# Kernel optimization log

Measured on AMD Instinct MI355X. Metric: run time of the kernel, lower is better.

The kernel has to match this reference:

```python
import jax, jax.numpy as jnp
import numpy as np

NUM_HEADS = 8
NORM_GROUPS = 32
EPS = 1e-5


def setup_inputs() -> dict:
    key = jax.random.key(0)
    k1, k2, k3 = jax.random.split(key, 3)
    b, c, h, w = 16, 256, 64, 64
    x = jax.random.normal(k1, (b, c, h, w), dtype=jnp.float32)
    gn_w = jnp.ones((c,), dtype=jnp.float32)
    gn_b = jnp.zeros((c,), dtype=jnp.float32)
    # 1x1 convs == channel matmuls; init like torch (kaiming-ish scale)
    w_qkv = jax.random.normal(k2, (3 * c, c), dtype=jnp.float32) / np.sqrt(c)
    w_proj = jax.random.normal(k3, (c, c), dtype=jnp.float32) / np.sqrt(c)
    b_proj = jnp.zeros((c,), dtype=jnp.float32)
    return {"x": x, "gn_w": gn_w, "gn_b": gn_b, "w_qkv": w_qkv,
            "w_proj": w_proj, "b_proj": b_proj}


def reference(x, gn_w, gn_b, w_qkv, w_proj, b_proj):
    b, c, h, w = x.shape
    H = NUM_HEADS
    d = c // H
    n = h * w
    # GroupNorm over (channels_per_group, h, w)
    xg = x.reshape(b, NORM_GROUPS, -1)
    mu = jnp.mean(xg, axis=-1, keepdims=True)
    var = jnp.mean(jnp.square(xg - mu), axis=-1, keepdims=True)
    xn = ((xg - mu) * jax.lax.rsqrt(var + EPS)).reshape(b, c, h, w)
    xn = xn * gn_w[None, :, None, None] + gn_b[None, :, None, None]
    # 1x1 conv -> (b, 3c, h, w); channel layout is (qkv, heads, d)
    qkv = jnp.einsum('oc,bchw->bohw', w_qkv, xn)
    qkv = qkv.reshape(b, 3, H, d, n)
    q, k, v = qkv[:, 0], qkv[:, 1], qkv[:, 2]  # each (b, H, d, n)
    k = jax.nn.softmax(k, axis=-1)
    # linear attention: small (d x d) state per head
    att = jnp.einsum('bhdn,bhen->bhde', k, v)
    out = jnp.einsum('bhde,bhdn->bhen', att, q)  # (b, H, d, n)
    out = out.reshape(b, c, h, w)
    return jnp.einsum('oc,bchw->bohw', w_proj, out) + b_proj[None, :, None, None]
```

## Files before the change

kernel.cpp:

```cpp
#include <hip/hip_runtime.h>
#include <stdint.h>

#define BATCH 16
#define CCH   256
#define NSP   4096

typedef unsigned short u16;
typedef short  short8 __attribute__((ext_vector_type(8)));
typedef float  f32x4  __attribute__((ext_vector_type(4)));

__device__ __forceinline__ float bf2f(u16 h) {
  union { unsigned int u; float f; } x; x.u = ((unsigned int)h) << 16; return x.f;
}
__device__ __forceinline__ u16 f2bf(float f) {
  union { float f; unsigned int u; } x; x.f = f;
  unsigned int r = 0x7fffu + ((x.u >> 16) & 1u);
  return (u16)((x.u + r) >> 16);
}

#define GLB(p) ((__attribute__((address_space(1))) void*)(p))
#define LDSP(p) ((__attribute__((address_space(3))) void*)(p))

__global__ __launch_bounds__(256) void prep_kernel(const float* __restrict__ x,
                                                   const float* __restrict__ wq,
                                                   const float* __restrict__ wp,
                                                   float2* __restrict__ stats,
                                                   float* __restrict__ att4,
                                                   u16* __restrict__ wbf,
                                                   u16* __restrict__ wqT) {
  __shared__ float red[8];
  __shared__ u16 ls[64][72];
  const int blk = blockIdx.x, tid = threadIdx.x;
  if (blk < 512) {
    {
      float* az = att4 + (size_t)blk * 264;
      for (int i = tid; i < 264; i += 256) az[i] = 0.f;
    }
    const float4* xv = (const float4*)(x + (size_t)blk * 32768);
    float s = 0.f, ss = 0.f;
    for (int i = tid; i < 8192; i += 256) {
      float4 u = xv[i];
      s  += u.x + u.y + u.z + u.w;
      ss += u.x * u.x + u.y * u.y + u.z * u.z + u.w * u.w;
    }
#pragma unroll
    for (int off = 32; off > 0; off >>= 1) {
      s  += __shfl_down(s, off);
      ss += __shfl_down(ss, off);
    }
    const int wave = tid >> 6, lane = tid & 63;
    if (lane == 0) { red[wave * 2] = s; red[wave * 2 + 1] = ss; }
    __syncthreads();
    if (tid == 0) {
      const float S  = red[0] + red[2] + red[4] + red[6];
      const float SS = red[1] + red[3] + red[5] + red[7];
      const float mean = S * (1.f / 32768.f);
      const float var  = SS * (1.f / 32768.f) - mean * mean;
      stats[blk] = make_float2(mean, rsqrtf(var + 1e-5f));
    }
  } else if (blk < 768) {
    const int i = ((blk - 512) * 256 + tid) * 4;
    float4 v = (i < 196608) ? *(const float4*)(wq + i)
                            : *(const float4*)(wp + (i - 196608));
    ushort4 o;
    o.x = f2bf(v.x); o.y = f2bf(v.y); o.z = f2bf(v.z); o.w = f2bf(v.w);
    *(ushort4*)(wbf + i) = o;
  } else {
    const int t2 = blk - 768;
    const int c0 = (t2 & 3) * 64, r0 = (t2 >> 2) * 64;
#pragma unroll
    for (int j = 0; j < 4; ++j) {
      const int row = j * 16 + (tid >> 4), col = (tid & 15) * 4;
      float4 u = *(const float4*)(wq + (r0 + row) * 256 + c0 + col);
      ls[row][col]     = f2bf(u.x);
      ls[row][col + 1] = f2bf(u.y);
      ls[row][col + 2] = f2bf(u.z);
      ls[row][col + 3] = f2bf(u.w);
    }
    __syncthreads();
#pragma unroll
    for (int j = 0; j < 2; ++j) {
      const int crow = j * 32 + (tid >> 3), d8 = (tid & 7) * 8;
      u16 tmp[8];
#pragma unroll
      for (int k = 0; k < 8; ++k) tmp[k] = ls[d8 + k][crow];
      *(uint4*)(wqT + (c0 + crow) * 256 + r0 + d8) = *(uint4*)tmp;
    }
  }
}

__global__ __launch_bounds__(256) void gn_apply_t(const float* __restrict__ x,
                                                  const float* __restrict__ gw,
                                                  const float* __restrict__ gb,
                                                  const float2* __restrict__ stats,
                                                  u16* __restrict__ xnT) {
  __shared__ u16 ls[64][72];
  const int b = blockIdx.z, c0 = blockIdx.y * 64, n0 = blockIdx.x * 64;
  const int tid = threadIdx.x;
#pragma unroll
  for (int r = 0; r < 4; ++r) {
    const int cc = (tid >> 4) + r * 16;
    const int nn = (tid & 15) * 4;
    const int c = c0 + cc;
    const float2 st = stats[b * 32 + (c >> 3)];
    const float wv = gw[c] * st.y;
    const float bv = gb[c] - st.x * wv;
    float4 u = *(const float4*)(x + ((size_t)b * CCH + c) * NSP + n0 + nn);
    ushort4 o;
    o.x = f2bf(u.x * wv + bv);
    o.y = f2bf(u.y * wv + bv);
    o.z = f2bf(u.z * wv + bv);
    o.w = f2bf(u.w * wv + bv);
    *(ushort4*)&ls[cc][nn] = o;
  }
  __syncthreads();
#pragma unroll
  for (int p = 0; p < 2; ++p) {
    const int idx = tid + p * 256;
    const int nn = idx >> 3;
    const int cb = (idx & 7) * 8;
    u16 tmp[8];
#pragma unroll
    for (int j = 0; j < 8; ++j) tmp[j] = ls[cb + j][nn];
    *(uint4*)(xnT + ((size_t)b * NSP + n0 + nn) * CCH + c0 + cb) = *(uint4*)tmp;
  }
}

template <int OUTF32>
__global__ __launch_bounds__(256) void gemm_mfma(const u16* __restrict__ A,
                                                 const u16* __restrict__ Bt,
                                                 const float* __restrict__ bias,
                                                 void* __restrict__ Cm, int M,
                                                 int aBatch, long btStride, int ldc) {
  __shared__ __align__(16) u16 smem[17408];
  const int tid = threadIdx.x, wave = tid >> 6, lane = tid & 63;
  const int n0 = blockIdx.x * 128, m0 = blockIdx.y * 128, bz = blockIdx.z;
  const u16* Ab = A + (size_t)bz * aBatch;
  const u16* Bb = Bt + (size_t)bz * btStride;

  const int lrow = lane >> 3;
  const int kcl  = ((lane & 7) ^ lrow) * 8;
  const u16* pA[4]; const u16* pB[4];
#pragma unroll
  for (int j = 0; j < 4; ++j) {
    const int row = j * 32 + wave * 8 + lrow;
    pA[j] = Ab + (size_t)(m0 + row) * CCH + kcl;
    pB[j] = Bb + (size_t)(n0 + row) * CCH + kcl;
  }
  u16* lA = smem;
  u16* lB = smem + 8192;

  const int wm = wave >> 1, wn = wave & 1;
  f32x4 acc[4][4];
#pragma unroll
  for (int i = 0; i < 4; ++i)
#pragma unroll
    for (int j = 0; j < 4; ++j) acc[i][j] = (f32x4){0.f, 0.f, 0.f, 0.f};

  for (int it = 0; it < 4; ++it) {
#pragma unroll
    for (int j = 0; j < 4; ++j) {
      __builtin_amdgcn_global_load_lds(GLB(pA[j]), LDSP(lA + (j * 256 + wave * 64) * 8), 16, 0, 0);
      __builtin_amdgcn_global_load_lds(GLB(pB[j]), LDSP(lB + (j * 256 + wave * 64) * 8), 16, 0, 0);
      pA[j] += 64; pB[j] += 64;
    }
    __syncthreads();
#pragma unroll
    for (int w = 0; w < 2; ++w) {
      const int kcf = w * 4 + (lane >> 4);
      short8 af[4], bfr[4];
#pragma unroll
      for (int mt = 0; mt < 4; ++mt) {
        const int row = wm * 64 + mt * 16 + (lane & 15);
        af[mt] = *(const short8*)&lA[(row * 8 + (kcf ^ (row & 7))) * 8];
      }
#pragma unroll
      for (int nt = 0; nt < 4; ++nt) {
        const int row = wn * 64 + nt * 16 + (lane & 15);
        bfr[nt] = *(const short8*)&lB[(row * 8 + (kcf ^ (row & 7))) * 8];
      }
#pragma unroll
      for (int mt = 0; mt < 4; ++mt)
#pragma unroll
        for (int nt = 0; nt < 4; ++nt)
          acc[mt][nt] = __builtin_amdgcn_mfma_f32_16x16x32_bf16(af[mt], bfr[nt], acc[mt][nt], 0, 0, 0);
    }
    __syncthreads();
  }

  if (!OUTF32) {
    u16* cl = smem;
#pragma unroll
    for (int mt = 0; mt < 4; ++mt)
#pragma unroll
      for (int nt = 0; nt < 4; ++nt)
#pragma unroll
        for (int r = 0; r < 4; ++r) {
          const int row = wm * 64 + mt * 16 + (lane >> 4) * 4 + r;
          const int col = wn * 64 + nt * 16 + (lane & 15);
          cl[row * 136 + col] = f2bf(acc[mt][nt][r]);
        }
    __syncthreads();
    u16* C = (u16*)Cm + (size_t)bz * (size_t)M * ldc;
#pragma unroll
    for (int j = 0; j < 8; ++j) {
      const int idx = tid + j * 256;
      const int row = idx >> 4, chunk = idx & 15;
      *(uint4*)(C + (size_t)(m0 + row) * ldc + n0 + chunk * 8) =
          *(const uint4*)&cl[row * 136 + chunk * 8];
    }
  } else {
    float* clf = (float*)smem;
    float* C = (float*)Cm + (size_t)bz * (size_t)M * ldc;
#pragma unroll
    for (int pass = 0; pass < 2; ++pass) {
      if (wm == pass) {
#pragma unroll
        for (int mt = 0; mt < 4; ++mt)
#pragma unroll
          for (int nt = 0; nt < 4; ++nt)
#pragma unroll
            for (int r = 0; r < 4; ++r) {
              const int rl = mt * 16 + (lane >> 4) * 4 + r;
              const int col = wn * 64 + nt * 16 + (lane & 15);
              clf[rl * 132 + col] = acc[mt][nt][r] + bias[m0 + pass * 64 + rl];
            }
      }
      __syncthreads();
#pragma unroll
      for (int j = 0; j < 8; ++j) {
        const int idx = tid + j * 256;
        const int row = idx >> 5, chunk = idx & 31;
        *(float4*)(C + (size_t)(m0 + pass * 64 + row) * ldc + n0 + chunk * 4) =
            *(const float4*)&clf[row * 132 + chunk * 4];
      }
      __syncthreads();
    }
  }
}

__global__ __launch_bounds__(256, 4) void gemm_kv_att(const u16* __restrict__ A,
                                                      const u16* __restrict__ Bt,
                                                      float* __restrict__ att4) {
  __shared__ __align__(16) u16 smem[17408];
  const int tid = threadIdx.x, wave = tid >> 6, lane = tid & 63;
  const int n0 = blockIdx.x * 128, hg = blockIdx.y, b = blockIdx.z;
  const u16* Bb = Bt + (size_t)b * (size_t)NSP * CCH;

  const int lrow = lane >> 3;
  const int kcl  = ((lane & 7) ^ lrow) * 8;
  const u16* pA[4]; const u16* pB[4];
#pragma unroll
  for (int j = 0; j < 4; ++j) {
    const int arow = 256 + (j >> 1) * 256 + hg * 64 + (j & 1) * 32 + wave * 8 + lrow;
    pA[j] = A  + (size_t)arow * CCH + kcl;
    pB[j] = Bb + (size_t)(n0 + j * 32 + wave * 8 + lrow) * CCH + kcl;
  }
  u16* lA = smem;
  u16* lB = smem + 8192;

  const int wm = wave >> 1, wn = wave & 1;
  f32x4 acc[4][4];
#pragma unroll
  for (int i = 0; i < 4; ++i)
#pragma unroll
    for (int j = 0; j < 4; ++j) acc[i][j] = (f32x4){0.f, 0.f, 0.f, 0.f};

  for (int it = 0; it < 4; ++it) {
#pragma unroll
    for (int j = 0; j < 4; ++j) {
      __builtin_amdgcn_global_load_lds(GLB(pA[j]), LDSP(lA + (j * 256 + wave * 64) * 8), 16, 0, 0);
      __builtin_amdgcn_global_load_lds(GLB(pB[j]), LDSP(lB + (j * 256 + wave * 64) * 8), 16, 0, 0);
      pA[j] += 64; pB[j] += 64;
    }
    __syncthreads();
#pragma unroll
    for (int w = 0; w < 2; ++w) {
      const int kcf = w * 4 + (lane >> 4);
      short8 af[4], bfr[4];
#pragma unroll
      for (int mt = 0; mt < 4; ++mt) {
        const int row = wm * 64 + mt * 16 + (lane & 15);
        af[mt] = *(const short8*)&lA[(row * 8 + (kcf ^ (row & 7))) * 8];
      }
#pragma unroll
      for (int nt = 0; nt < 4; ++nt) {
        const int row = wn * 64 + nt * 16 + (lane & 15);
        bfr[nt] = *(const short8*)&lB[(row * 8 + (kcf ^ (row & 7))) * 8];
      }
#pragma unroll
      for (int mt = 0; mt < 4; ++mt)
#pragma unroll
        for (int nt = 0; nt < 4; ++nt)
          acc[mt][nt] = __builtin_amdgcn_mfma_f32_16x16x32_bf16(af[mt], bfr[nt], acc[mt][nt], 0, 0, 0);
    }
    __syncthreads();
  }

  u16* clK = smem;
  u16* clV = smem + 8704;
  {
    const int rbase = (lane >> 4) * 4;
    if (wm == 0) {
#pragma unroll
      for (int mt = 0; mt < 4; ++mt)
#pragma unroll
        for (int nt = 0; nt < 4; ++nt)
#pragma unroll
          for (int r = 0; r < 4; ++r) {
            const int row = mt * 16 + rbase + r;
            const int col = wn * 64 + nt * 16 + (lane & 15);
            clK[row * 136 + col] = f2bf(__expf(acc[mt][nt][r]));
          }
    } else {
#pragma unroll
      for (int mt = 0; mt < 4; ++mt)
#pragma unroll
        for (int nt = 0; nt < 4; ++nt)
#pragma unroll
          for (int r = 0; r < 4; ++r) {
            const int row = mt * 16 + rbase + r;
            const int col = wn * 64 + nt * 16 + (lane & 15);
            clV[row * 136 + col] = f2bf(acc[mt][nt][r]);
          }
    }
  }
  __syncthreads();

  const int hh = wave >> 1, nhalf = wave & 1;
  const int bh = b * 8 + hg * 2 + hh;
  f32x4 a2[2][2], al[2];
#pragma unroll
  for (int i = 0; i < 2; ++i) {
    al[i] = (f32x4){0.f, 0.f, 0.f, 0.f};
#pragma unroll
    for (int j = 0; j < 2; ++j) a2[i][j] = (f32x4){0.f, 0.f, 0.f, 0.f};
  }
  short8 ones;
#pragma unroll
  for (int j = 0; j < 8; ++j) ones[j] = (short)0x3F80;

  const int rr = lane & 15, cc8 = (lane >> 4) * 8;
#pragma unroll
  for (int c = 0; c < 2; ++c) {
    const int n = (nhalf * 2 + c) * 32 + cc8;
    short8 ek0 = *(const short8*)&clK[(hh * 32 + rr) * 136 + n];
    short8 ek1 = *(const short8*)&clK[(hh * 32 + 16 + rr) * 136 + n];
    short8 v0  = *(const short8*)&clV[(hh * 32 + rr) * 136 + n];
    short8 v1  = *(const short8*)&clV[(hh * 32 + 16 + rr) * 136 + n];
    a2[0][0] = __builtin_amdgcn_mfma_f32_16x16x32_bf16(ek0, v0, a2[0][0], 0, 0, 0);
    a2[0][1] = __builtin_amdgcn_mfma_f32_16x16x32_bf16(ek0, v1, a2[0][1], 0, 0, 0);
    a2[1][0] = __builtin_amdgcn_mfma_f32_16x16x32_bf16(ek1, v0, a2[1][0], 0, 0, 0);
    a2[1][1] = __builtin_amdgcn_mfma_f32_16x16x32_bf16(ek1, v1, a2[1][1], 0, 0, 0);
    al[0]    = __builtin_amdgcn_mfma_f32_16x16x32_bf16(ek0, ones, al[0], 0, 0, 0);
    al[1]    = __builtin_amdgcn_mfma_f32_16x16x32_bf16(ek1, ones, al[1], 0, 0, 0);
  }
  __syncthreads();

  float* red  = (float*)smem;
  float* redl = red + 2176;
  const int dq = (lane >> 4) * 4;
  if (nhalf == 1) {
#pragma unroll
    for (int dh = 0; dh < 2; ++dh) {
#pragma unroll
      for (int eh = 0; eh < 2; ++eh)
#pragma unroll
        for (int j = 0; j < 4; ++j)
          red[hh * 1088 + (dh * 16 + dq + j) * 34 + eh * 16 + rr] = a2[dh][eh][j];
      if (rr == 0)
#pragma unroll
        for (int j = 0; j < 4; ++j) redl[hh * 32 + dh * 16 + dq + j] = al[dh][j];
    }
  }
  __syncthreads();
  if (nhalf == 0) {
    float* ap = att4 + (size_t)bh * 1056;
#pragma unroll
    for (int dh = 0; dh < 2; ++dh) {
#pragma unroll
      for (int eh = 0; eh < 2; ++eh)
#pragma unroll
        for (int j = 0; j < 4; ++j) {
          const int d = dh * 16 + dq + j, e = eh * 16 + rr;
          atomicAdd(&ap[d * 32 + e], a2[dh][eh][j] + red[hh * 1088 + d * 34 + e]);
        }
      if (rr == 0)
#pragma unroll
        for (int j = 0; j < 4; ++j) {
          const int d = dh * 16 + dq + j;
          atomicAdd(&ap[1024 + d], al[dh][j] + redl[hh * 32 + d]);
        }
    }
  }
}

__global__ __launch_bounds__(256) void w2_kernel(const u16* __restrict__ wp_bf,
                                                 const float* __restrict__ att4,
                                                 u16* __restrict__ W2) {
  const int b = blockIdx.x >> 4;
  const int o0 = (blockIdx.x & 15) * 16;
  const int tid = threadIdx.x;
  const int h = tid >> 5, d = tid & 31;
  const float* ap = att4 + ((size_t)b * 8 + h) * 1056;
  const float linv = 1.f / ap[1024 + d];
  float as[32];
#pragma unroll
  for (int e = 0; e < 32; ++e) as[e] = ap[d * 32 + e] * linv;
  u16* w2p = W2 + (size_t)b * 65536;
  for (int oi = 0; oi < 16; ++oi) {
    const int o = o0 + oi;
    const uint4* wr = (const uint4*)(wp_bf + o * 256 + h * 32);
    float acc = 0.f;
#pragma unroll
    for (int j = 0; j < 4; ++j) {
      uint4 u = wr[j];
      const u16* w8 = (const u16*)&u;
#pragma unroll
      for (int t = 0; t < 8; ++t) acc += bf2f(w8[t]) * as[j * 8 + t];
    }
    w2p[o * 256 + tid] = f2bf(acc);
  }
}

extern "C" void kernel_launch(void* const* d_in, const int* in_sizes, int n_in,
                              void* d_out, int out_size, void* d_ws, size_t ws_size,
                              hipStream_t stream) {
  const float* x      = (const float*)d_in[0];
  const float* gn_w   = (const float*)d_in[1];
  const float* gn_b   = (const float*)d_in[2];
  const float* w_qkv  = (const float*)d_in[3];
  const float* w_proj = (const float*)d_in[4];
  const float* b_proj = (const float*)d_in[5];
  float* out = (float*)d_out;

  char* ws = (char*)d_ws;
  u16*    xnT   = (u16*)ws;
  u16*    wbf   = (u16*)(ws + 33554432ull);
  u16*    wqT   = (u16*)(ws + 34078720ull);
  u16*    W2    = (u16*)(ws + 34209792ull);
  u16*    W3    = (u16*)(ws + 36306944ull);
  float*  att4  = (float*)(ws + 38404096ull);
  float2* stats = (float2*)(ws + 38944768ull);
  u16* wq_bf = wbf;
  u16* wp_bf = wbf + 196608;

  prep_kernel<<<784, 256, 0, stream>>>(x, w_qkv, w_proj, stats, att4, wbf, wqT);
  gn_apply_t<<<dim3(64, 4, 16), 256, 0, stream>>>(x, gn_w, gn_b, stats, xnT);
  gemm_kv_att<<<dim3(32, 4, 16), 256, 0, stream>>>(wq_bf, xnT, att4);
  w2_kernel<<<256, 256, 0, stream>>>(wp_bf, att4, W2);
  gemm_mfma<0><<<dim3(2, 2, 16), 256, 0, stream>>>(W2, wqT, nullptr, W3,
                                                   CCH, 65536, 0L, CCH);
  gemm_mfma<1><<<dim3(32, 2, 16), 256, 0, stream>>>(W3, xnT, b_proj, out,
                                                    CCH, 65536, (long)NSP * CCH, NSP);
}
```

Before: 208.1 us.

## Fuse all stages into one persistent cooperative kernel with grid syncs

Wraps each stage body in a device function and adds a cooperative persistent kernel that runs all six phases in sequence, separated by grid-wide barriers. Blocks loop over each phase's tiles with a fixed grid of 1024. The goal is to remove kernel launch overhead and the inter-kernel drain gaps. In exchange it adds grid-sync cost, pins the occupancy assumption to 4 blocks per CU, and leaves most of the grid idle during the small phases. Non-cooperative launches remain as a fallback.

New measurement: 213.2 us. 1.02x slower.

```diff
diff --git a/kernel.cpp b/kernel.cpp
--- a/kernel.cpp
+++ b/kernel.cpp
@@ -1,5 +1,8 @@
 #include <hip/hip_runtime.h>
+#include <hip/hip_cooperative_groups.h>
 #include <stdint.h>
+
+namespace cg = cooperative_groups;
 
 #define BATCH 16
 #define CCH   256
@@ -21,17 +24,12 @@
 #define GLB(p) ((__attribute__((address_space(1))) void*)(p))
 #define LDSP(p) ((__attribute__((address_space(3))) void*)(p))
 
-__global__ __launch_bounds__(256) void prep_kernel(const float* __restrict__ x,
-                                                   const float* __restrict__ wq,
-                                                   const float* __restrict__ wp,
-                                                   float2* __restrict__ stats,
-                                                   float* __restrict__ att4,
-                                                   u16* __restrict__ wbf,
-                                                   u16* __restrict__ wqT) {
-  __shared__ float red[8];
-  __shared__ u16 ls[64][72];
-  const int blk = blockIdx.x, tid = threadIdx.x;
+__device__ __forceinline__ void prep_body(int blk, int tid, const float* x,
+                                          const float* wq, const float* wp,
+                                          float2* stats, float* att4,
+                                          u16* wbf, u16* wqT, u16* smem) {
   if (blk < 512) {
+    float* red = (float*)(smem + 4608);
     {
       float* az = att4 + (size_t)blk * 264;
       for (int i = tid; i < 264; i += 256) az[i] = 0.f;
@@ -66,6 +64,7 @@
     o.x = f2bf(v.x); o.y = f2bf(v.y); o.z = f2bf(v.z); o.w = f2bf(v.w);
     *(ushort4*)(wbf + i) = o;
   } else {
+    u16 (*ls)[72] = (u16(*)[72])smem;
     const int t2 = blk - 768;
     const int c0 = (t2 & 3) * 64, r0 = (t2 >> 2) * 64;
 #pragma unroll
@@ -89,14 +88,12 @@
   }
 }
 
-__global__ __launch_bounds__(256) void gn_apply_t(const float* __restrict__ x,
-                                                  const float* __restrict__ gw,
-                                                  const float* __restrict__ gb,
-                                                  const float2* __restrict__ stats,
-                                                  u16* __restrict__ xnT) {
-  __shared__ u16 ls[64][72];
-  const int b = blockIdx.z, c0 = blockIdx.y * 64, n0 = blockIdx.x * 64;
-  const int tid = threadIdx.x;
+__device__ __forceinline__ void gn_apply_body(int n0t, int c0t, int b, int tid,
+                                              const float* x, const float* gw,
+                                              const float* gb, const float2* stats,
+                                              u16* xnT, u16* smem) {
+  u16 (*ls)[72] = (u16(*)[72])smem;
+  const int c0 = c0t * 64, n0 = n0t * 64;
 #pragma unroll
   for (int r = 0; r < 4; ++r) {
     const int cc = (tid >> 4) + r * 16;
@@ -127,14 +124,12 @@
 }
 
 template <int OUTF32>
-__global__ __launch_bounds__(256) void gemm_mfma(const u16* __restrict__ A,
-                                                 const u16* __restrict__ Bt,
-                                                 const float* __restrict__ bias,
-                                                 void* __restrict__ Cm, int M,
-                                                 int aBatch, long btStride, int ldc) {
-  __shared__ __align__(16) u16 smem[17408];
-  const int tid = threadIdx.x, wave = tid >> 6, lane = tid & 63;
-  const int n0 = blockIdx.x * 128, m0 = blockIdx.y * 128, bz = blockIdx.z;
+__device__ __forceinline__ void gemm_body(const u16* A, const u16* Bt,
+                                          const float* bias, void* Cm, int M,
+                                          int aBatch, long btStride, int ldc,
+                                          int n0, int m0, int bz,
+                                          int tid, u16* smem) {
+  const int wave = tid >> 6, lane = tid & 63;
   const u16* Ab = A + (size_t)bz * aBatch;
   const u16* Bb = Bt + (size_t)bz * btStride;
 
@@ -239,12 +234,11 @@
   }
 }
 
-__global__ __launch_bounds__(256, 4) void gemm_kv_att(const u16* __restrict__ A,
-                                                      const u16* __restrict__ Bt,
-                                                      float* __restrict__ att4) {
-  __shared__ __align__(16) u16 smem[17408];
-  const int tid = threadIdx.x, wave = tid >> 6, lane = tid & 63;
-  const int n0 = blockIdx.x * 128, hg = blockIdx.y, b = blockIdx.z;
+__device__ __forceinline__ void kv_att_body(int nblk, int hg, int b, int tid,
+                                            const u16* A, const u16* Bt,
+                                            float* att4, u16* smem) {
+  const int wave = tid >> 6, lane = tid & 63;
+  const int n0 = nblk * 128;
   const u16* Bb = Bt + (size_t)b * (size_t)NSP * CCH;
 
   const int lrow = lane >> 3;
@@ -395,12 +389,10 @@
   }
 }
 
-__global__ __launch_bounds__(256) void w2_kernel(const u16* __restrict__ wp_bf,
-                                                 const float* __restrict__ att4,
-                                                 u16* __restrict__ W2) {
-  const int b = blockIdx.x >> 4;
-  const int o0 = (blockIdx.x & 15) * 16;
-  const int tid = threadIdx.x;
+__device__ __forceinline__ void w2_body(int blk, int tid, const u16* wp_bf,
+                                        const float* att4, u16* W2) {
+  const int b = blk >> 4;
+  const int o0 = (blk & 15) * 16;
   const int h = tid >> 5, d = tid & 31;
   const float* ap = att4 + ((size_t)b * 8 + h) * 1056;
   const float linv = 1.f / ap[1024 + d];
@@ -420,6 +412,105 @@
       for (int t = 0; t < 8; ++t) acc += bf2f(w8[t]) * as[j * 8 + t];
     }
     w2p[o * 256 + tid] = f2bf(acc);
+  }
+}
+
+__global__ __launch_bounds__(256) void prep_kernel(const float* __restrict__ x,
+                                                   const float* __restrict__ wq,
+                                                   const float* __restrict__ wp,
+                                                   float2* __restrict__ stats,
+                                                   float* __restrict__ att4,
+                                                   u16* __restrict__ wbf,
+                                                   u16* __restrict__ wqT) {
+  __shared__ __align__(16) u16 smem[17408];
+  prep_body(blockIdx.x, threadIdx.x, x, wq, wp, stats, att4, wbf, wqT, smem);
+}
+
+__global__ __launch_bounds__(256) void gn_apply_t(const float* __restrict__ x,
+                                                  const float* __restrict__ gw,
+                                                  const float* __restrict__ gb,
+                                                  const float2* __restrict__ stats,
+                                                  u16* __restrict__ xnT) {
+  __shared__ __align__(16) u16 smem[17408];
+  gn_apply_body(blockIdx.x, blockIdx.y, blockIdx.z, threadIdx.x, x, gw, gb, stats, xnT, smem);
+}
+
+template <int OUTF32>
+__global__ __launch_bounds__(256) void gemm_mfma(const u16* __restrict__ A,
+                                                 const u16* __restrict__ Bt,
+                                                 const float* __restrict__ bias,
+                                                 void* __restrict__ Cm, int M,
+                                                 int aBatch, long btStride, int ldc) {
+  __shared__ __align__(16) u16 smem[17408];
+  gemm_body<OUTF32>(A, Bt, bias, Cm, M, aBatch, btStride, ldc,
+                    blockIdx.x * 128, blockIdx.y * 128, blockIdx.z,
+                    threadIdx.x, smem);
+}
+
+__global__ __launch_bounds__(256, 4) void gemm_kv_att(const u16* __restrict__ A,
+                                                      const u16* __restrict__ Bt,
+                                                      float* __restrict__ att4) {
+  __shared__ __align__(16) u16 smem[17408];
+  kv_att_body(blockIdx.x, blockIdx.y, blockIdx.z, threadIdx.x, A, Bt, att4, smem);
+}
+
+__global__ __launch_bounds__(256) void w2_kernel(const u16* __restrict__ wp_bf,
+                                                 const float* __restrict__ att4,
+                                                 u16* __restrict__ W2) {
+  w2_body(blockIdx.x, threadIdx.x, wp_bf, att4, W2);
+}
+
+__global__ __launch_bounds__(256, 4) void fused_all(
+    const float* __restrict__ x, const float* __restrict__ gn_w,
+    const float* __restrict__ gn_b, const float* __restrict__ w_qkv,
+    const float* __restrict__ w_proj, const float* __restrict__ b_proj,
+    float* __restrict__ out, u16* __restrict__ xnT, u16* __restrict__ wbf,
+    u16* __restrict__ wqT, u16* __restrict__ W2, u16* __restrict__ W3,
+    float* __restrict__ att4, float2* __restrict__ stats) {
+  __shared__ __align__(16) u16 smem[17408];
+  cg::grid_group grid = cg::this_grid();
+  const int bid = blockIdx.x, tid = threadIdx.x;
+  const int g = gridDim.x;
+  const u16* wq_bf = wbf;
+  const u16* wp_bf = wbf + 196608;
+
+  for (int i = bid; i < 784; i += g) {
+    prep_body(i, tid, x, w_qkv, w_proj, stats, att4, wbf, wqT, smem);
+    __syncthreads();
+  }
+  __threadfence();
+  grid.sync();
+
+  for (int it = bid; it < 4096; it += g) {
+    gn_apply_body(it & 63, (it >> 6) & 3, it >> 8, tid, x, gn_w, gn_b, stats, xnT, smem);
+    __syncthreads();
+  }
+  __threadfence();
+  grid.sync();
+
+  for (int it = bid; it < 2048; it += g) {
+    kv_att_body(it & 31, (it >> 5) & 3, it >> 7, tid, wq_bf, xnT, att4, smem);
+    __syncthreads();
+  }
+  __threadfence();
+  grid.sync();
+
+  for (int i = bid; i < 256; i += g) w2_body(i, tid, wp_bf, att4, W2);
+  __threadfence();
+  grid.sync();
+
+  for (int i = bid; i < 64; i += g) {
+    gemm_body<0>(W2, wqT, nullptr, W3, CCH, 65536, 0L, CCH,
+                 (i & 1) * 128, ((i >> 1) & 1) * 128, i >> 2, tid, smem);
+    __syncthreads();
+  }
+  __threadfence();
+  grid.sync();
+
+  for (int it = bid; it < 1024; it += g) {
+    gemm_body<1>(W3, xnT, b_proj, out, CCH, 65536, (long)NSP * CCH, NSP,
+                 (it & 31) * 128, ((it >> 5) & 1) * 128, it >> 6, tid, smem);
+    __syncthreads();
   }
 }
 
@@ -445,6 +536,25 @@
   u16* wq_bf = wbf;
   u16* wp_bf = wbf + 196608;
 
+  static int coop_state = 0;
+  if (coop_state == 0) {
+    int occ = 0;
+    hipError_t e = hipOccupancyMaxActiveBlocksPerMultiprocessor(
+        &occ, (const void*)fused_all, 256, 0);
+    coop_state = (e == hipSuccess && occ >= 4) ? 1 : -1;
+  }
+  if (coop_state == 1) {
+    void* args[14] = {
+      (void*)&x, (void*)&gn_w, (void*)&gn_b, (void*)&w_qkv, (void*)&w_proj,
+      (void*)&b_proj, (void*)&out, (void*)&xnT, (void*)&wbf, (void*)&wqT,
+      (void*)&W2, (void*)&W3, (void*)&att4, (void*)&stats
+    };
+    hipError_t e = hipLaunchCooperativeKernel((void*)fused_all, dim3(1024),
+                                              dim3(256), args, 0, stream);
+    if (e == hipSuccess) return;
+    coop_state = -1;
+  }
+
   prep_kernel<<<784, 256, 0, stream>>>(x, w_qkv, w_proj, stats, att4, wbf, wqT);
   gn_apply_t<<<dim3(64, 4, 16), 256, 0, stream>>>(x, gn_w, gn_b, stats, xnT);
   gemm_kv_att<<<dim3(32, 4, 16), 256, 0, stream>>>(wq_bf, xnT, att4);
```

## Fuse W2 computation into the W3 GEMM kernel, removing a launch

Applied to the files above, without the earlier changes.

Merges w2_kernel and the bf16-output gemm into one w23_kernel. Each block normalizes the per-head attention state into LDS, builds its 128-row slice of W2 with MFMA directly in LDS, then multiplies by wqT to produce W3. This removes one kernel launch and the W2 round trip through global memory. In exchange each block recomputes its W2 rows, which duplicates that work across the column blocks, and the kernel uses much more shared memory.

New measurement: 214.3 us. 1.03x slower.

```diff
diff --git a/kernel.cpp b/kernel.cpp
--- a/kernel.cpp
+++ b/kernel.cpp
@@ -126,12 +126,11 @@
   }
 }
 
-template <int OUTF32>
-__global__ __launch_bounds__(256) void gemm_mfma(const u16* __restrict__ A,
-                                                 const u16* __restrict__ Bt,
-                                                 const float* __restrict__ bias,
-                                                 void* __restrict__ Cm, int M,
-                                                 int aBatch, long btStride, int ldc) {
+__global__ __launch_bounds__(256) void gemm_f32(const u16* __restrict__ A,
+                                                const u16* __restrict__ Bt,
+                                                const float* __restrict__ bias,
+                                                float* __restrict__ Cm, int M,
+                                                int aBatch, long btStride, int ldc) {
   __shared__ __align__(16) u16 smem[17408];
   const int tid = threadIdx.x, wave = tid >> 6, lane = tid & 63;
   const int n0 = blockIdx.x * 128, m0 = blockIdx.y * 128, bz = blockIdx.z;
@@ -188,54 +187,31 @@
     __syncthreads();
   }
 
-  if (!OUTF32) {
-    u16* cl = smem;
-#pragma unroll
-    for (int mt = 0; mt < 4; ++mt)
-#pragma unroll
-      for (int nt = 0; nt < 4; ++nt)
-#pragma unroll
-        for (int r = 0; r < 4; ++r) {
-          const int row = wm * 64 + mt * 16 + (lane >> 4) * 4 + r;
-          const int col = wn * 64 + nt * 16 + (lane & 15);
-          cl[row * 136 + col] = f2bf(acc[mt][nt][r]);
-        }
-    __syncthreads();
-    u16* C = (u16*)Cm + (size_t)bz * (size_t)M * ldc;
+  float* clf = (float*)smem;
+  float* C = Cm + (size_t)bz * (size_t)M * ldc;
+#pragma unroll
+  for (int pass = 0; pass < 2; ++pass) {
+    if (wm == pass) {
+#pragma unroll
+      for (int mt = 0; mt < 4; ++mt)
+#pragma unroll
+        for (int nt = 0; nt < 4; ++nt)
+#pragma unroll
+          for (int r = 0; r < 4; ++r) {
+            const int rl = mt * 16 + (lane >> 4) * 4 + r;
+            const int col = wn * 64 + nt * 16 + (lane & 15);
+            clf[rl * 132 + col] = acc[mt][nt][r] + bias[m0 + pass * 64 + rl];
+          }
+    }
+    __syncthreads();
 #pragma unroll
     for (int j = 0; j < 8; ++j) {
       const int idx = tid + j * 256;
-      const int row = idx >> 4, chunk = idx & 15;
-      *(uint4*)(C + (size_t)(m0 + row) * ldc + n0 + chunk * 8) =
-          *(const uint4*)&cl[row * 136 + chunk * 8];
-    }
-  } else {
-    float* clf = (float*)smem;
-    float* C = (float*)Cm + (size_t)bz * (size_t)M * ldc;
-#pragma unroll
-    for (int pass = 0; pass < 2; ++pass) {
-      if (wm == pass) {
-#pragma unroll
-        for (int mt = 0; mt < 4; ++mt)
-#pragma unroll
-          for (int nt = 0; nt < 4; ++nt)
-#pragma unroll
-            for (int r = 0; r < 4; ++r) {
-              const int rl = mt * 16 + (lane >> 4) * 4 + r;
-              const int col = wn * 64 + nt * 16 + (lane & 15);
-              clf[rl * 132 + col] = acc[mt][nt][r] + bias[m0 + pass * 64 + rl];
-            }
-      }
-      __syncthreads();
-#pragma unroll
-      for (int j = 0; j < 8; ++j) {
-        const int idx = tid + j * 256;
-        const int row = idx >> 5, chunk = idx & 31;
-        *(float4*)(C + (size_t)(m0 + pass * 64 + row) * ldc + n0 + chunk * 4) =
-            *(const float4*)&clf[row * 132 + chunk * 4];
-      }
-      __syncthreads();
-    }
+      const int row = idx >> 5, chunk = idx & 31;
+      *(float4*)(C + (size_t)(m0 + pass * 64 + row) * ldc + n0 + chunk * 4) =
+          *(const float4*)&clf[row * 132 + chunk * 4];
+    }
+    __syncthreads();
   }
 }
 
@@ -395,31 +371,118 @@
   }
 }
 
-__global__ __launch_bounds__(256) void w2_kernel(const u16* __restrict__ wp_bf,
-                                                 const float* __restrict__ att4,
-                                                 u16* __restrict__ W2) {
-  const int b = blockIdx.x >> 4;
-  const int o0 = (blockIdx.x & 15) * 16;
-  const int tid = threadIdx.x;
-  const int h = tid >> 5, d = tid & 31;
-  const float* ap = att4 + ((size_t)b * 8 + h) * 1056;
-  const float linv = 1.f / ap[1024 + d];
-  float as[32];
-#pragma unroll
-  for (int e = 0; e < 32; ++e) as[e] = ap[d * 32 + e] * linv;
-  u16* w2p = W2 + (size_t)b * 65536;
-  for (int oi = 0; oi < 16; ++oi) {
-    const int o = o0 + oi;
-    const uint4* wr = (const uint4*)(wp_bf + o * 256 + h * 32);
-    float acc = 0.f;
+__global__ __launch_bounds__(256) void w23_kernel(const u16* __restrict__ wp_bf,
+                                                  const u16* __restrict__ wqT,
+                                                  const float* __restrict__ att4,
+                                                  u16* __restrict__ W3) {
+  __shared__ __align__(16) u16 smem[58880];
+  const int tid = threadIdx.x, wave = tid >> 6, lane = tid & 63;
+  const int n0 = blockIdx.x * 128, m0 = blockIdx.y * 128, b = blockIdx.z;
+
+  u16*   lA  = smem;
+  float* asb = (float*)(smem + 33792);
+  u16*   lB  = smem + 50688;
+
+  {
+    const float* ab = att4 + (size_t)b * 8 * 1056;
+    for (int i = tid; i < 8192; i += 256) {
+      const int h = i >> 10, d = (i >> 5) & 31, e = i & 31;
+      asb[h * 1056 + d * 33 + e] = ab[h * 1056 + d * 32 + e] / ab[h * 1056 + 1024 + d];
+    }
+  }
+  __syncthreads();
+
+  {
+    const int r16 = lane & 15, e0 = (lane >> 4) * 8;
+#pragma unroll
+    for (int hh = 0; hh < 2; ++hh) {
+      const int h = wave * 2 + hh;
+#pragma unroll
+      for (int nt = 0; nt < 2; ++nt) {
+        const float* bp = asb + h * 1056 + (nt * 16 + r16) * 33 + e0;
+        short8 bfr;
+#pragma unroll
+        for (int j = 0; j < 8; ++j) bfr[j] = (short)f2bf(bp[j]);
+#pragma unroll
+        for (int mt = 0; mt < 8; ++mt) {
+          const int orow = mt * 16 + r16;
+          short8 af = *(const short8*)(wp_bf + (size_t)(m0 + orow) * 256 + h * 32 + e0);
+          f32x4 c = __builtin_amdgcn_mfma_f32_16x16x32_bf16(af, bfr, (f32x4){0.f,0.f,0.f,0.f}, 0, 0, 0);
+#pragma unroll
+          for (int r = 0; r < 4; ++r) {
+            const int o = mt * 16 + (lane >> 4) * 4 + r;
+            const int d2 = h * 32 + nt * 16 + r16;
+            lA[o * 264 + d2] = f2bf(c[r]);
+          }
+        }
+      }
+    }
+  }
+  __syncthreads();
+
+  const int lrow = lane >> 3;
+  const int kcl  = ((lane & 7) ^ lrow) * 8;
+  const u16* pB[4];
+#pragma unroll
+  for (int j = 0; j < 4; ++j)
+    pB[j] = wqT + (size_t)(n0 + j * 32 + wave * 8 + lrow) * 256 + kcl;
+
+  const int wm = wave >> 1, wn = wave & 1;
+  f32x4 acc[4][4];
+#pragma unroll
+  for (int i = 0; i < 4; ++i)
+#pragma unroll
+    for (int j = 0; j < 4; ++j) acc[i][j] = (f32x4){0.f, 0.f, 0.f, 0.f};
+
+  for (int it = 0; it < 4; ++it) {
 #pragma unroll
     for (int j = 0; j < 4; ++j) {
-      uint4 u = wr[j];
-      const u16* w8 = (const u16*)&u;
-#pragma unroll
-      for (int t = 0; t < 8; ++t) acc += bf2f(w8[t]) * as[j * 8 + t];
-    }
-    w2p[o * 256 + tid] = f2bf(acc);
+      __builtin_amdgcn_global_load_lds(GLB(pB[j]), LDSP(lB + (j * 256 + wave * 64) * 8), 16, 0, 0);
+      pB[j] += 64;
+    }
+    __syncthreads();
+#pragma unroll
+    for (int w = 0; w < 2; ++w) {
+      const int kcf = w * 4 + (lane >> 4);
+      short8 af[4], bfr[4];
+#pragma unroll
+      for (int mt = 0; mt < 4; ++mt) {
+        const int row = wm * 64 + mt * 16 + (lane & 15);
+        af[mt] = *(const short8*)&lA[row * 264 + it * 64 + kcf * 8];
+      }
+#pragma unroll
+      for (int nt = 0; nt < 4; ++nt) {
+        const int row = wn * 64 + nt * 16 + (lane & 15);
+        bfr[nt] = *(const short8*)&lB[(row * 8 + (kcf ^ (row & 7))) * 8];
+      }
+#pragma unroll
+      for (int mt = 0; mt < 4; ++mt)
+#pragma unroll
+        for (int nt = 0; nt < 4; ++nt)
+          acc[mt][nt] = __builtin_amdgcn_mfma_f32_16x16x32_bf16(af[mt], bfr[nt], acc[mt][nt], 0, 0, 0);
+    }
+    __syncthreads();
+  }
+
+  u16* cl = smem + 33792;
+#pragma unroll
+  for (int mt = 0; mt < 4; ++mt)
+#pragma unroll
+    for (int nt = 0; nt < 4; ++nt)
+#pragma unroll
+      for (int r = 0; r < 4; ++r) {
+        const int row = wm * 64 + mt * 16 + (lane >> 4) * 4 + r;
+        const int col = wn * 64 + nt * 16 + (lane & 15);
+        cl[row * 136 + col] = f2bf(acc[mt][nt][r]);
+      }
+  __syncthreads();
+  u16* C = W3 + (size_t)b * 65536;
+#pragma unroll
+  for (int j = 0; j < 8; ++j) {
+    const int idx = tid + j * 256;
+    const int row = idx >> 4, chunk = idx & 15;
+    *(uint4*)(C + (size_t)(m0 + row) * 256 + n0 + chunk * 8) =
+        *(const uint4*)&cl[row * 136 + chunk * 8];
   }
 }
 
@@ -438,7 +501,6 @@
   u16*    xnT   = (u16*)ws;
   u16*    wbf   = (u16*)(ws + 33554432ull);
   u16*    wqT   = (u16*)(ws + 34078720ull);
-  u16*    W2    = (u16*)(ws + 34209792ull);
   u16*    W3    = (u16*)(ws + 36306944ull);
   float*  att4  = (float*)(ws + 38404096ull);
   float2* stats = (float2*)(ws + 38944768ull);
@@ -448,9 +510,7 @@
   prep_kernel<<<784, 256, 0, stream>>>(x, w_qkv, w_proj, stats, att4, wbf, wqT);
   gn_apply_t<<<dim3(64, 4, 16), 256, 0, stream>>>(x, gn_w, gn_b, stats, xnT);
   gemm_kv_att<<<dim3(32, 4, 16), 256, 0, stream>>>(wq_bf, xnT, att4);
-  w2_kernel<<<256, 256, 0, stream>>>(wp_bf, att4, W2);
-  gemm_mfma<0><<<dim3(2, 2, 16), 256, 0, stream>>>(W2, wqT, nullptr, W3,
-                                                   CCH, 65536, 0L, CCH);
-  gemm_mfma<1><<<dim3(32, 2, 16), 256, 0, stream>>>(W3, xnT, b_proj, out,
-                                                    CCH, 65536, (long)NSP * CCH, NSP);
-}
+  w23_kernel<<<dim3(2, 2, 16), 256, 0, stream>>>(wp_bf, wqT, att4, W3);
+  gemm_f32<<<dim3(32, 2, 16), 256, 0, stream>>>(W3, xnT, b_proj, out,
+                                                CCH, 65536, (long)NSP * CCH, NSP);
+}
```
